# Kernel optimization log

Measured on AMD Instinct MI355X. Metric: run time of the kernel, lower is better.

## Reference

```python
import jax, jax.numpy as jnp
import numpy as np

NC = 80
CONF = 0.25
IOU_T = 0.45
MAX_DET = 100
ATTN_RES = 14
NUM_BASE = 5
TOPK = 1024          # candidate pre-filter (EfficientNMS-style)
SCALE = 0.25         # spatial_scale of ROIAlign


def setup_inputs() -> dict:
    key = jax.random.key(0)
    k1, k2, k3, k4 = jax.random.split(key, 4)
    B, A = 4, 25200
    test = jax.random.uniform(k1, (B, A, 5 + NC), dtype=jnp.float32)
    # scale boxes to image coords: cx,cy in [0,608), w,h in [0,120)
    box_scale = jnp.concatenate([jnp.array([608., 608., 120., 120.], jnp.float32),
                                 jnp.ones(1 + NC, jnp.float32)])
    test = test * box_scale
    attn = jax.random.normal(k2, (B, A, NUM_BASE * ATTN_RES * ATTN_RES), dtype=jnp.float32)
    bases = jax.random.normal(k3, (B, NUM_BASE - 1, 160, 160), dtype=jnp.float32)
    sem = jax.random.normal(k4, (B, 1, 160, 160), dtype=jnp.float32)
    return {"test": test, "attn": attn, "bases": bases, "sem": sem}


def _iou_matrix(b):
    # b: [K,4] xyxy
    area = jnp.clip(b[:, 2] - b[:, 0], 0) * jnp.clip(b[:, 3] - b[:, 1], 0)
    lt = jnp.maximum(b[:, None, :2], b[None, :, :2])
    rb = jnp.minimum(b[:, None, 2:], b[None, :, 2:])
    wh = jnp.clip(rb - lt, 0)
    inter = wh[..., 0] * wh[..., 1]
    return inter / (area[:, None] + area[None, :] - inter + 1e-9)


def _nms_single(boxes, scores):
    # boxes [A,4], scores [A,NC]. Class-aware greedy NMS over top-K candidates.
    flat = scores.reshape(-1)
    flat = jnp.where(flat > CONF, flat, -jnp.inf)
    top_s, top_i = jax.lax.top_k(flat, TOPK)
    anchor = top_i // NC
    cls = top_i % NC
    cb = boxes[anchor]                                   # [K,4]
    sup = (_iou_matrix(cb) > IOU_T) & (cls[:, None] == cls[None, :])

    def step(valid, _):
        s = jnp.where(valid, top_s, -jnp.inf)
        j = jnp.argmax(s)
        ok = jnp.isfinite(s[j])
        nv = (valid & ~sup[j]).at[j].set(False)
        return jnp.where(ok, nv, valid), (j, ok)

    _, (sel, selok) = jax.lax.scan(step, jnp.isfinite(top_s), None, length=MAX_DET)
    dboxes = jnp.where(selok[:, None], cb[sel], 0.)
    dscores = jnp.where(selok, top_s[sel], 0.)
    dcls = jnp.where(selok, cls[sel], 0).astype(jnp.int32)
    didx = jnp.where(selok, anchor[sel], 0).astype(jnp.int32)
    return selok.sum().astype(jnp.int32), dboxes, dscores, dcls, didx


def _roi_align(feat, rois, bidx, oh, ow, scale):
    # feat [B,C,H,W], rois [N,4] xyxy (input coords), half_pixel transform,
    # avg mode, 1 sample/bin (adaptive ratio = 1 here since bins < 1 px).
    N = rois.shape[0]
    B, C, H, W = feat.shape
    x1 = rois[:, 0] * scale - 0.5
    y1 = rois[:, 1] * scale - 0.5
    x2 = rois[:, 2] * scale - 0.5
    y2 = rois[:, 3] * scale - 0.5
    ys = y1[:, None] + (jnp.arange(oh, dtype=feat.dtype) + 0.5) * ((y2 - y1) / oh)[:, None]
    xs = x1[:, None] + (jnp.arange(ow, dtype=feat.dtype) + 0.5) * ((x2 - x1) / ow)[:, None]

    def axis(coord, dim):
        valid = (coord > -1.0) & (coord < dim)
        c = jnp.clip(coord, 0.0, dim - 1.0)
        lo = jnp.floor(c)
        hi = jnp.clip(lo + 1, 0, dim - 1)
        return lo.astype(jnp.int32), hi.astype(jnp.int32), c - lo, valid

    y0, y1i, wy, vy = axis(ys, H)
    x0, x1i, wx, vx = axis(xs, W)
    featn = feat[bidx]                                   # [N,C,H,W]
    n = jnp.arange(N)[:, None, None]

    def g(Y, X):  # -> [N,oh,ow,C]
        return featn[n, :, Y[:, :, None], X[:, None, :]]

    wy_ = wy[:, :, None, None]
    wx_ = wx[:, None, :, None]
    val = (g(y0, x0) * (1 - wy_) * (1 - wx_) + g(y0, x1i) * (1 - wy_) * wx_
           + g(y1i, x0) * wy_ * (1 - wx_) + g(y1i, x1i) * wy_ * wx_)
    val = jnp.where((vy[:, :, None] & vx[:, None, :])[..., None], val, 0.)
    return jnp.transpose(val, (0, 3, 1, 2))                # [N,C,oh,ow]


def _forward(test, attn, bases_in, sem):
    bases = jnp.concatenate([bases_in, sem], axis=1)       # [B,5,H,W]
    conv = jnp.array([[1, 0, 1, 0], [0, 1, 0, 1],
                      [-0.5, 0, 0.5, 0], [0, -0.5, 0, 0.5]], test.dtype)
    boxes = test[:, :, :4] @ conv                          # cxcywh -> xyxy
    scores = test[:, :, 5:5 + NC] * test[:, :, 4:5]
    _, dboxes, dscores, dcls, didx = jax.vmap(_nms_single)(boxes, scores)
    B, P, H, W = bases.shape
    bidx = jnp.repeat(jnp.arange(B), MAX_DET)              # [B*D]
    box_i = didx.reshape(-1)
    sel_boxes = boxes[bidx, box_i]                         # [N,4]
    sel_masks = attn[bidx, box_i]                          # [N,980]
    pooled = _roi_align(bases, sel_boxes, bidx, H, W, SCALE)  # [N,5,H,W]
    coeffs = sel_masks.reshape(-1, NUM_BASE, ATTN_RES, ATTN_RES)
    coeffs = jax.image.resize(coeffs, (coeffs.shape[0], NUM_BASE, H, W), 'linear')
    coeffs = jax.nn.softmax(coeffs, axis=1)
    masks = jax.nn.sigmoid((pooled * coeffs).sum(axis=1).reshape(B, MAX_DET, H * W))
    return jnp.concatenate([dboxes, dscores[..., None],
                            dcls.astype(test.dtype)[..., None], masks], axis=-1)


def reference(test, attn, bases, sem):
    return _forward(test, attn, bases, sem)
```

## Files before the change

### kernel.cpp

```cpp
#include <hip/hip_runtime.h>
#include <stdint.h>

#define B_   4
#define A_   25200
#define NC_  80
#define ROW_ 85
#define ATT_ 980
#define MAXDET_ 100
#define TOPK_ 1024
#define CAP_  4096
#define OUTSTRIDE_ 25606
#define HW_ 160
#define HWHW_ 25600
#define CONF_ 0.25f
#define IOUT_ 0.45f

#define WS_HIST 0
#define WS_CNT  4096
#define WS_TB   4160
#define WS_NTOP 4224
#define WS_CAND 8192
#define WS_TOPV 139264
#define WS_TOPA 155648
#define WS_TOPC 172032
#define WS_CB   188416
#define WS_SUP  253952
#define WS_DETA 778240

typedef unsigned long long u64;
typedef unsigned u32;

__global__ void k_clear(char* w) {
    int i = blockIdx.x * 256 + threadIdx.x;
    if (i < 1028) ((u32*)w)[i] = 0u;
}

__global__ void k_hist(const float* __restrict__ test, char* __restrict__ w) {
    int b = blockIdx.y;
    __shared__ u32 h[256];
    if (threadIdx.x < 256) h[threadIdx.x] = 0u;
    __syncthreads();
    const int total = A_ * NC_;
    for (int e = blockIdx.x * 256 + threadIdx.x; e < total; e += 128 * 256) {
        u32 a = (u32)e / 80u;
        u32 c = (u32)e - a * 80u;
        const float* row = test + ((size_t)b * A_ + a) * ROW_;
        float s = row[5 + c] * row[4];
        if (s > CONF_) {
            u32 key = __float_as_uint(s);
            int wb = (int)(key >> 17) - 7936;
            wb = wb < 0 ? 0 : (wb > 255 ? 255 : wb);
            atomicAdd(&h[wb], 1u);
        }
    }
    __syncthreads();
    u32* hist = (u32*)(w + WS_HIST);
    if (threadIdx.x < 256 && h[threadIdx.x]) atomicAdd(&hist[b * 256 + threadIdx.x], h[threadIdx.x]);
}

__global__ void k_thresh(char* w) {
    if (threadIdx.x < B_) {
        int b = threadIdx.x;
        const u32* h = (const u32*)(w + WS_HIST) + b * 256;
        u32 cum = 0; int wtb = 0;
        for (int i = 255; i >= 0; --i) {
            cum += h[i];
            if (cum >= TOPK_) { wtb = i; break; }
        }
        ((int*)(w + WS_TB))[b] = wtb;
    }
}

__global__ void k_collect(const float* __restrict__ test, char* __restrict__ w) {
    int b = blockIdx.y;
    int wtb = ((const int*)(w + WS_TB))[b];
    u32* cnt = (u32*)(w + WS_CNT);
    u64* cand = (u64*)(w + WS_CAND);
    const int total = A_ * NC_;
    for (int e = blockIdx.x * 256 + threadIdx.x; e < total; e += 128 * 256) {
        u32 a = (u32)e / 80u;
        u32 c = (u32)e - a * 80u;
        const float* row = test + ((size_t)b * A_ + a) * ROW_;
        float s = row[5 + c] * row[4];
        if (s > CONF_) {
            u32 key = __float_as_uint(s);
            int wb = (int)(key >> 17) - 7936;
            wb = wb < 0 ? 0 : (wb > 255 ? 255 : wb);
            if (wb >= wtb) {
                u32 pos = atomicAdd(&cnt[b], 1u);
                if (pos < CAP_)
                    cand[(size_t)b * CAP_ + pos] = ((u64)key << 32) | (u64)(0xFFFFFFFFu - (u32)e);
            }
        }
    }
}

__global__ __launch_bounds__(1024) void k_sort(const float* __restrict__ test, char* __restrict__ w) {
    int b = blockIdx.x;
    __shared__ u64 sm[CAP_];
    u32 cnt = ((const u32*)(w + WS_CNT))[b];
    int n = cnt < CAP_ ? (int)cnt : CAP_;
    const u64* cand = (const u64*)(w + WS_CAND) + (size_t)b * CAP_;
    for (int i = threadIdx.x; i < CAP_; i += 1024) sm[i] = (i < n) ? cand[i] : 0ull;
    __syncthreads();
    for (int k = 2; k <= CAP_; k <<= 1) {
        for (int j = k >> 1; j > 0; j >>= 1) {
            for (int t = threadIdx.x; t < CAP_; t += 1024) {
                int ixj = t ^ j;
                if (ixj > t) {
                    u64 a = sm[t], c = sm[ixj];
                    bool desc = ((t & k) == 0);
                    if (desc ? (a < c) : (a > c)) { sm[t] = c; sm[ixj] = a; }
                }
            }
            __syncthreads();
        }
    }
    int ntop = n < TOPK_ ? n : TOPK_;
    if (threadIdx.x == 0) ((int*)(w + WS_NTOP))[b] = ntop;
    if (threadIdx.x < TOPK_) {
        int i = threadIdx.x;
        float* topv = (float*)(w + WS_TOPV);
        int* topa = (int*)(w + WS_TOPA);
        int* topc = (int*)(w + WS_TOPC);
        float4* cb = (float4*)(w + WS_CB);
        if (i < ntop) {
            u64 v = sm[i];
            u32 key = (u32)(v >> 32);
            u32 idx = 0xFFFFFFFFu - (u32)(v & 0xFFFFFFFFull);
            u32 anchor = idx / 80u;
            u32 cls = idx - anchor * 80u;
            const float* tr = test + ((size_t)b * A_ + anchor) * ROW_;
            float cx = tr[0], cy = tr[1], ww = tr[2], hh = tr[3];
            float4 box;
            box.x = cx - 0.5f * ww; box.y = cy - 0.5f * hh;
            box.z = cx + 0.5f * ww; box.w = cy + 0.5f * hh;
            topv[b * TOPK_ + i] = __uint_as_float(key);
            topa[b * TOPK_ + i] = (int)anchor;
            topc[b * TOPK_ + i] = (int)cls;
            cb[b * TOPK_ + i] = box;
        } else {
            topv[b * TOPK_ + i] = 0.f;
            topa[b * TOPK_ + i] = 0;
            topc[b * TOPK_ + i] = 0;
            cb[b * TOPK_ + i] = make_float4(0.f, 0.f, 0.f, 0.f);
        }
    }
}

__device__ __forceinline__ bool sup_pair(float4 a, float4 b, int ca, int cbb) {
#pragma clang fp contract(off)
    if (ca != cbb) return false;
    float areaA = fmaxf(a.z - a.x, 0.f) * fmaxf(a.w - a.y, 0.f);
    float areaB = fmaxf(b.z - b.x, 0.f) * fmaxf(b.w - b.y, 0.f);
    float ltx = fmaxf(a.x, b.x), lty = fmaxf(a.y, b.y);
    float rbx = fminf(a.z, b.z), rby = fminf(a.w, b.w);
    float iw = fmaxf(rbx - ltx, 0.f), ih = fmaxf(rby - lty, 0.f);
    float inter = iw * ih;
    float iou = inter / (((areaA + areaB) - inter) + 1e-9f);
    return iou > IOUT_;
}

__global__ void k_sup(char* __restrict__ w) {
    int b = blockIdx.y;
    int t = blockIdx.x * 256 + threadIdx.x;
    int row = t >> 4, chunk = t & 15;
    const float4* cb = (const float4*)(w + WS_CB) + (size_t)b * TOPK_;
    const int* topc = (const int*)(w + WS_TOPC) + (size_t)b * TOPK_;
    float4 rb = cb[row];
    int rc = topc[row];
    u64 bits = 0ull;
    int base = chunk * 64;
    for (int cc = 0; cc < 64; ++cc) {
        if (sup_pair(rb, cb[base + cc], rc, topc[base + cc])) bits |= (1ull << cc);
    }
    ((u64*)(w + WS_SUP))[((size_t)b * TOPK_ + row) * 16 + chunk] = bits;
}

__global__ void k_nms(char* __restrict__ w, float* __restrict__ out) {
    int b = blockIdx.x;
    int lane = threadIdx.x;
    int ntop = ((const int*)(w + WS_NTOP))[b];
    const u64* sup = (const u64*)(w + WS_SUP);
    __shared__ int selA[MAXDET_];
    __shared__ int okA[MAXDET_];
    u32 valid = 0u;
    for (int t = 0; t < 16; ++t)
        if (lane * 16 + t < ntop) valid |= (1u << t);
    for (int k = 0; k < MAXDET_; ++k) {
        u64 bal = __ballot(valid != 0u);
        if (bal == 0ull) {
            if (lane == 0) { selA[k] = 0; okA[k] = 0; }
            continue;
        }
        int L = __ffsll(bal) - 1;
        u32 vL = (u32)__shfl((int)valid, L);
        int j = L * 16 + (__ffs(vL & 0xFFFFu) - 1);
        u64 chunk = sup[((size_t)b * TOPK_ + j) * 16 + (lane >> 2)];
        u32 s16 = (u32)(chunk >> ((lane & 3) * 16)) & 0xFFFFu;
        valid &= ~s16;
        if (lane == L) valid &= ~(1u << (j & 15));
        if (lane == 0) { selA[k] = j; okA[k] = 1; }
    }
    __syncthreads();
    const float* topv = (const float*)(w + WS_TOPV) + (size_t)b * TOPK_;
    const int* topa = (const int*)(w + WS_TOPA) + (size_t)b * TOPK_;
    const int* topc = (const int*)(w + WS_TOPC) + (size_t)b * TOPK_;
    const float4* cb = (const float4*)(w + WS_CB) + (size_t)b * TOPK_;
    int* deta = (int*)(w + WS_DETA);
    for (int k = lane; k < MAXDET_; k += 64) {
        int ok = okA[k], s = selA[k];
        float b0 = 0, b1 = 0, b2 = 0, b3 = 0, sc = 0; int cls_ = 0, anc = 0;
        if (ok) {
            float4 bb = cb[s];
            b0 = bb.x; b1 = bb.y; b2 = bb.z; b3 = bb.w;
            sc = topv[s]; cls_ = topc[s]; anc = topa[s];
        }
        size_t o = ((size_t)(b * MAXDET_ + k)) * OUTSTRIDE_;
        out[o + 0] = b0; out[o + 1] = b1; out[o + 2] = b2; out[o + 3] = b3;
        out[o + 4] = sc; out[o + 5] = (float)cls_;
        deta[b * MAXDET_ + k] = anc;
    }
}

__global__ __launch_bounds__(256) void k_mask(const float* __restrict__ test, const float* __restrict__ attn,
                       const float* __restrict__ bases, const float* __restrict__ sem,
                       const char* __restrict__ w, float* __restrict__ out) {
    int roi = blockIdx.x;
    int by = blockIdx.y;
    int b = roi / MAXDET_;
    int anchor = ((const int*)(w + WS_DETA))[roi];
    const float* t = test + ((size_t)b * A_ + anchor) * ROW_;
    float cx = t[0], cy = t[1], ww = t[2], hh = t[3];
    float bx1 = cx - 0.5f * ww, by1 = cy - 0.5f * hh;
    float bx2 = cx + 0.5f * ww, by2 = cy + 0.5f * hh;
    float rx1 = bx1 * 0.25f - 0.5f, ry1 = by1 * 0.25f - 0.5f;
    float rx2 = bx2 * 0.25f - 0.5f, ry2 = by2 * 0.25f - 0.5f;
    float xstep = (rx2 - rx1) / 160.f, ystep = (ry2 - ry1) / 160.f;

    __shared__ float XR[5 * 8 * 160];
    __shared__ float CXR[5 * 4 * 160];
    __shared__ float att[ATT_];
    __shared__ int   sxlo[HW_], sxhi[HW_];
    __shared__ float sxw[HW_], sxvF[HW_];
    __shared__ int   rzlo[HW_];
    __shared__ float rzw[HW_];
    __shared__ int   yloA[20], yhiA[20], cyloA[20], cyhiA[20];
    __shared__ float ywA[20], cwyA[20], yvF[20];
    __shared__ int rminS, crminS;

    int tid = threadIdx.x;
    const float* arow = attn + ((size_t)b * A_ + anchor) * ATT_;
    for (int i = tid; i < ATT_; i += 256) att[i] = arow[i];
    if (tid < HW_) {
        float coord = rx1 + (tid + 0.5f) * xstep;
        sxvF[tid] = (coord > -1.0f && coord < 160.0f) ? 1.f : 0.f;
        float c = fminf(fmaxf(coord, 0.f), 159.f);
        float lo = floorf(c);
        sxlo[tid] = (int)lo; sxhi[tid] = min((int)lo + 1, 159); sxw[tid] = c - lo;
        float f = (tid + 0.5f) * (14.f / 160.f) - 0.5f;
        float rc = fminf(fmaxf(f, 0.f), 13.f);
        float rlo = floorf(rc);
        rzlo[tid] = (int)rlo; rzw[tid] = rc - rlo;
    }
    __syncthreads();
    if (tid < 20) {
        int yg = by * 20 + tid;
        float coord = ry1 + (yg + 0.5f) * ystep;
        yvF[tid] = (coord > -1.0f && coord < 160.0f) ? 1.f : 0.f;
        float c = fminf(fmaxf(coord, 0.f), 159.f);
        float lo = floorf(c);
        yloA[tid] = (int)lo; yhiA[tid] = min((int)lo + 1, 159); ywA[tid] = c - lo;
        cyloA[tid] = rzlo[yg]; cwyA[tid] = rzw[yg]; cyhiA[tid] = min(rzlo[yg] + 1, 13);
    }
    __syncthreads();
    if (tid == 0) {
        int rm = 159, cm = 13;
        for (int i = 0; i < 20; ++i) { rm = min(rm, yloA[i]); cm = min(cm, cyloA[i]); }
        rminS = rm; crminS = cm;
    }
    __syncthreads();
    int rmin = rminS, crmin = crminS;

    const float* bp[5];
    bp[0] = bases + ((size_t)b * 4 + 0) * HWHW_;
    bp[1] = bases + ((size_t)b * 4 + 1) * HWHW_;
    bp[2] = bases + ((size_t)b * 4 + 2) * HWHW_;
    bp[3] = bases + ((size_t)b * 4 + 3) * HWHW_;
    bp[4] = sem + (size_t)b * HWHW_;

    for (int idx = tid; idx < 5 * 8 * 160; idx += 256) {
        int c = idx / (8 * 160);
        int rem = idx - c * (8 * 160);
        int r = rem / 160;
        int x = rem - r * 160;
        int row = min(rmin + r, 159);
        const float* pb = bp[c] + row * 160;
        float wx = sxw[x];
        XR[idx] = pb[sxlo[x]] * (1.f - wx) + pb[sxhi[x]] * wx;
    }
    for (int idx = tid; idx < 5 * 4 * 160; idx += 256) {
        int c = idx / (4 * 160);
        int rem = idx - c * (4 * 160);
        int rr = rem / 160;
        int x = rem - rr * 160;
        int row = min(crmin + rr, 13);
        const float* pa = att + c * 196 + row * 14;
        int xl = rzlo[x]; int xh = min(xl + 1, 13); float wxc = rzw[x];
        CXR[idx] = pa[xl] * (1.f - wxc) + pa[xh] * wxc;
    }
    __syncthreads();

    size_t obase = (size_t)roi * OUTSTRIDE_ + 6 + (size_t)by * 20 * HW_;
    for (int g = tid; g < 800; g += 256) {
        int yl = g / 40;
        int x4 = (g - yl * 40) * 4;
        float wy = ywA[yl], vy = yvF[yl], cwy = cwyA[yl];
        int rlo = min(max(yloA[yl] - rmin, 0), 7);
        int rhi = min(max(yhiA[yl] - rmin, 0), 7);
        int clo = min(max(cyloA[yl] - crmin, 0), 3);
        int chi = min(max(cyhiA[yl] - crmin, 0), 3);
        float p4[5][4], cf4[5][4];
#pragma unroll
        for (int c = 0; c < 5; ++c) {
            float4 a = *(const float4*)&XR[(c * 8 + rlo) * 160 + x4];
            float4 bq = *(const float4*)&XR[(c * 8 + rhi) * 160 + x4];
            p4[c][0] = a.x * (1.f - wy) + bq.x * wy;
            p4[c][1] = a.y * (1.f - wy) + bq.y * wy;
            p4[c][2] = a.z * (1.f - wy) + bq.z * wy;
            p4[c][3] = a.w * (1.f - wy) + bq.w * wy;
            float4 ca = *(const float4*)&CXR[(c * 4 + clo) * 160 + x4];
            float4 cbq = *(const float4*)&CXR[(c * 4 + chi) * 160 + x4];
            cf4[c][0] = ca.x * (1.f - cwy) + cbq.x * cwy;
            cf4[c][1] = ca.y * (1.f - cwy) + cbq.y * cwy;
            cf4[c][2] = ca.z * (1.f - cwy) + cbq.z * cwy;
            cf4[c][3] = ca.w * (1.f - cwy) + cbq.w * cwy;
        }
        float4 vx4 = *(const float4*)&sxvF[x4];
        float vx[4] = { vx4.x, vx4.y, vx4.z, vx4.w };
        float res[4];
#pragma unroll
        for (int i = 0; i < 4; ++i) {
            float v = vx[i] * vy;
            float se = 0.f, dot = 0.f;
#pragma unroll
            for (int c = 0; c < 5; ++c) {
                float e = __expf(cf4[c][i]);
                se += e;
                dot += p4[c][i] * e;
            }
            float r = v * dot / se;
            res[i] = 1.f / (1.f + __expf(-r));
        }
        float2* o2 = (float2*)(out + obase + (size_t)yl * HW_ + x4);
        o2[0] = make_float2(res[0], res[1]);
        o2[1] = make_float2(res[2], res[3]);
    }
}

extern "C" void kernel_launch(void* const* d_in, const int* in_sizes, int n_in,
                              void* d_out, int out_size, void* d_ws, size_t ws_size,
                              hipStream_t stream) {
    const float* test = (const float*)d_in[0];
    const float* attn = (const float*)d_in[1];
    const float* bases = (const float*)d_in[2];
    const float* sem = (const float*)d_in[3];
    float* out = (float*)d_out;
    char* w = (char*)d_ws;

    k_clear<<<5, 256, 0, stream>>>(w);
    k_hist<<<dim3(128, B_), 256, 0, stream>>>(test, w);
    k_thresh<<<1, 64, 0, stream>>>(w);
    k_collect<<<dim3(128, B_), 256, 0, stream>>>(test, w);
    k_sort<<<B_, 1024, 0, stream>>>(test, w);
    k_sup<<<dim3(64, B_), 256, 0, stream>>>(w);
    k_nms<<<B_, 64, 0, stream>>>(w, out);
    k_mask<<<dim3(B_ * MAXDET_, 8), 256, 0, stream>>>(test, attn, bases, sem, w, out);
}
```

Before: 735.0 us.

## Split candidates into sure and boundary sets, sort only the boundary bucket

The threshold computation moves into the last block of the histogram kernel using a completion ticket, which removes one launch. Candidates strictly above the threshold bucket go to an unsorted 'sure' list, and only the boundary bucket is bitonic-sorted, padded to a power of two. Because the sure list is no longer ordered, the NMS kernel now finds the highest-scoring valid candidate with a wave-wide max reduction over packed keys instead of taking the first set bit. The mask kernel also shrinks its staged row buffer from 8 to 6 rows, which assumes that many rows cover each 20-row band.

```diff
diff --git a/kernel.cpp b/kernel.cpp
--- a/kernel.cpp
+++ b/kernel.cpp
@@ -8,7 +8,8 @@
 #define ATT_ 980
 #define MAXDET_ 100
 #define TOPK_ 1024
-#define CAP_  4096
+#define SURECAP_ 1024
+#define BNDCAP_  4096
 #define OUTSTRIDE_ 25606
 #define HW_ 160
 #define HWHW_ 25600
@@ -16,30 +17,78 @@
 #define IOUT_ 0.45f
 
 #define WS_HIST 0
-#define WS_CNT  4096
-#define WS_TB   4160
-#define WS_NTOP 4224
-#define WS_CAND 8192
-#define WS_TOPV 139264
-#define WS_TOPA 155648
-#define WS_TOPC 172032
-#define WS_CB   188416
-#define WS_SUP  253952
-#define WS_DETA 778240
+#define WS_DONE 4096
+#define WS_SCNT 4160
+#define WS_BCNT 4224
+#define WS_TB   4288
+#define WS_NTOP 4352
+#define WS_SURE 8192
+#define WS_BND  40960
+#define WS_KEY  172032
+#define WS_TOPV 204800
+#define WS_TOPA 221184
+#define WS_TOPC 237568
+#define WS_CB   253952
+#define WS_SUP  319488
+#define WS_DETA 843776
 
 typedef unsigned long long u64;
 typedef unsigned u32;
 
+__device__ __forceinline__ int bucket_of(u32 key) {
+    int wb = (int)(key >> 17) - 7936;
+    return wb < 0 ? 0 : (wb > 255 ? 255 : wb);
+}
+
 __global__ void k_clear(char* w) {
-    int i = blockIdx.x * 256 + threadIdx.x;
-    if (i < 1028) ((u32*)w)[i] = 0u;
+    for (int i = threadIdx.x; i < 1072; i += 1024) ((u32*)w)[i] = 0u;
 }
 
 __global__ void k_hist(const float* __restrict__ test, char* __restrict__ w) {
     int b = blockIdx.y;
     __shared__ u32 h[256];
+    __shared__ u32 ticket;
     if (threadIdx.x < 256) h[threadIdx.x] = 0u;
     __syncthreads();
+    const int total = A_ * NC_;
+    for (int e = blockIdx.x * 256 + threadIdx.x; e < total; e += 128 * 256) {
+        u32 a = (u32)e / 80u;
+        u32 c = (u32)e - a * 80u;
+        const float* row = test + ((size_t)b * A_ + a) * ROW_;
+        float s = row[5 + c] * row[4];
+        if (s > CONF_) atomicAdd(&h[bucket_of(__float_as_uint(s))], 1u);
+    }
+    __syncthreads();
+    u32* hist = (u32*)(w + WS_HIST);
+    if (threadIdx.x < 256 && h[threadIdx.x]) atomicAdd(&hist[b * 256 + threadIdx.x], h[threadIdx.x]);
+    __threadfence();
+    __syncthreads();
+    if (threadIdx.x == 0) ticket = atomicAdd((u32*)(w + WS_DONE), 1u);
+    __syncthreads();
+    if (ticket == 128u * B_ - 1u) {
+        __shared__ u32 hh[B_ * 256];
+        for (int i = threadIdx.x; i < B_ * 256; i += 256)
+            hh[i] = atomicAdd(&hist[i], 0u);
+        __syncthreads();
+        if (threadIdx.x < B_) {
+            const u32* hb = hh + threadIdx.x * 256;
+            u32 cum = 0; int wtb = 0;
+            for (int i = 255; i >= 0; --i) {
+                cum += hb[i];
+                if (cum >= TOPK_) { wtb = i; break; }
+            }
+            ((int*)(w + WS_TB))[threadIdx.x] = wtb;
+        }
+    }
+}
+
+__global__ void k_collect(const float* __restrict__ test, char* __restrict__ w) {
+    int b = blockIdx.y;
+    int wtb = ((const int*)(w + WS_TB))[b];
+    u32* scnt = (u32*)(w + WS_SCNT);
+    u32* bcnt = (u32*)(w + WS_BCNT);
+    u64* sure = (u64*)(w + WS_SURE);
+    u64* bnd = (u64*)(w + WS_BND);
     const int total = A_ * NC_;
     for (int e = blockIdx.x * 256 + threadIdx.x; e < total; e += 128 * 256) {
         u32 a = (u32)e / 80u;
@@ -48,64 +97,35 @@
         float s = row[5 + c] * row[4];
         if (s > CONF_) {
             u32 key = __float_as_uint(s);
-            int wb = (int)(key >> 17) - 7936;
-            wb = wb < 0 ? 0 : (wb > 255 ? 255 : wb);
-            atomicAdd(&h[wb], 1u);
-        }
-    }
-    __syncthreads();
-    u32* hist = (u32*)(w + WS_HIST);
-    if (threadIdx.x < 256 && h[threadIdx.x]) atomicAdd(&hist[b * 256 + threadIdx.x], h[threadIdx.x]);
-}
-
-__global__ void k_thresh(char* w) {
-    if (threadIdx.x < B_) {
-        int b = threadIdx.x;
-        const u32* h = (const u32*)(w + WS_HIST) + b * 256;
-        u32 cum = 0; int wtb = 0;
-        for (int i = 255; i >= 0; --i) {
-            cum += h[i];
-            if (cum >= TOPK_) { wtb = i; break; }
-        }
-        ((int*)(w + WS_TB))[b] = wtb;
-    }
-}
-
-__global__ void k_collect(const float* __restrict__ test, char* __restrict__ w) {
-    int b = blockIdx.y;
-    int wtb = ((const int*)(w + WS_TB))[b];
-    u32* cnt = (u32*)(w + WS_CNT);
-    u64* cand = (u64*)(w + WS_CAND);
-    const int total = A_ * NC_;
-    for (int e = blockIdx.x * 256 + threadIdx.x; e < total; e += 128 * 256) {
-        u32 a = (u32)e / 80u;
-        u32 c = (u32)e - a * 80u;
-        const float* row = test + ((size_t)b * A_ + a) * ROW_;
-        float s = row[5 + c] * row[4];
-        if (s > CONF_) {
-            u32 key = __float_as_uint(s);
-            int wb = (int)(key >> 17) - 7936;
-            wb = wb < 0 ? 0 : (wb > 255 ? 255 : wb);
+            int wb = bucket_of(key);
             if (wb >= wtb) {
-                u32 pos = atomicAdd(&cnt[b], 1u);
-                if (pos < CAP_)
-                    cand[(size_t)b * CAP_ + pos] = ((u64)key << 32) | (u64)(0xFFFFFFFFu - (u32)e);
+                u64 packed = ((u64)key << 32) | (u64)(0xFFFFFFFFu - (u32)e);
+                if (wb > wtb) {
+                    u32 pos = atomicAdd(&scnt[b], 1u);
+                    if (pos < SURECAP_) sure[(size_t)b * SURECAP_ + pos] = packed;
+                } else {
+                    u32 pos = atomicAdd(&bcnt[b], 1u);
+                    if (pos < BNDCAP_) bnd[(size_t)b * BNDCAP_ + pos] = packed;
+                }
             }
         }
     }
 }
 
-__global__ __launch_bounds__(1024) void k_sort(const float* __restrict__ test, char* __restrict__ w) {
+__global__ __launch_bounds__(1024) void k_bsort(const float* __restrict__ test, char* __restrict__ w) {
     int b = blockIdx.x;
-    __shared__ u64 sm[CAP_];
-    u32 cnt = ((const u32*)(w + WS_CNT))[b];
-    int n = cnt < CAP_ ? (int)cnt : CAP_;
-    const u64* cand = (const u64*)(w + WS_CAND) + (size_t)b * CAP_;
-    for (int i = threadIdx.x; i < CAP_; i += 1024) sm[i] = (i < n) ? cand[i] : 0ull;
-    __syncthreads();
-    for (int k = 2; k <= CAP_; k <<= 1) {
+    __shared__ u64 sm[BNDCAP_];
+    u32 ns_raw = ((const u32*)(w + WS_SCNT))[b];
+    u32 nb_raw = ((const u32*)(w + WS_BCNT))[b];
+    int ns = ns_raw < SURECAP_ ? (int)ns_raw : SURECAP_;
+    int nb = nb_raw < BNDCAP_ ? (int)nb_raw : BNDCAP_;
+    int p = 2; while (p < nb) p <<= 1;
+    const u64* bnd = (const u64*)(w + WS_BND) + (size_t)b * BNDCAP_;
+    for (int i = threadIdx.x; i < p; i += 1024) sm[i] = (i < nb) ? bnd[i] : 0ull;
+    __syncthreads();
+    for (int k = 2; k <= p; k <<= 1) {
         for (int j = k >> 1; j > 0; j >>= 1) {
-            for (int t = threadIdx.x; t < CAP_; t += 1024) {
+            for (int t = threadIdx.x; t < p; t += 1024) {
                 int ixj = t ^ j;
                 if (ixj > t) {
                     u64 a = sm[t], c = sm[ixj];
@@ -116,35 +136,39 @@
             __syncthreads();
         }
     }
-    int ntop = n < TOPK_ ? n : TOPK_;
+    int m = TOPK_ - ns; if (m > nb) m = nb;
+    int ntop = ns + m;
     if (threadIdx.x == 0) ((int*)(w + WS_NTOP))[b] = ntop;
-    if (threadIdx.x < TOPK_) {
-        int i = threadIdx.x;
-        float* topv = (float*)(w + WS_TOPV);
-        int* topa = (int*)(w + WS_TOPA);
-        int* topc = (int*)(w + WS_TOPC);
-        float4* cb = (float4*)(w + WS_CB);
-        if (i < ntop) {
-            u64 v = sm[i];
-            u32 key = (u32)(v >> 32);
-            u32 idx = 0xFFFFFFFFu - (u32)(v & 0xFFFFFFFFull);
-            u32 anchor = idx / 80u;
-            u32 cls = idx - anchor * 80u;
-            const float* tr = test + ((size_t)b * A_ + anchor) * ROW_;
-            float cx = tr[0], cy = tr[1], ww = tr[2], hh = tr[3];
-            float4 box;
-            box.x = cx - 0.5f * ww; box.y = cy - 0.5f * hh;
-            box.z = cx + 0.5f * ww; box.w = cy + 0.5f * hh;
-            topv[b * TOPK_ + i] = __uint_as_float(key);
-            topa[b * TOPK_ + i] = (int)anchor;
-            topc[b * TOPK_ + i] = (int)cls;
-            cb[b * TOPK_ + i] = box;
-        } else {
-            topv[b * TOPK_ + i] = 0.f;
-            topa[b * TOPK_ + i] = 0;
-            topc[b * TOPK_ + i] = 0;
-            cb[b * TOPK_ + i] = make_float4(0.f, 0.f, 0.f, 0.f);
-        }
+    const u64* sure = (const u64*)(w + WS_SURE) + (size_t)b * SURECAP_;
+    int i = threadIdx.x;
+    u64 v = 0ull;
+    if (i < ns) v = sure[i];
+    else if (i < ntop) v = sm[i - ns];
+    u64* keyo = (u64*)(w + WS_KEY);
+    float* topv = (float*)(w + WS_TOPV);
+    int* topa = (int*)(w + WS_TOPA);
+    int* topc = (int*)(w + WS_TOPC);
+    float4* cb = (float4*)(w + WS_CB);
+    keyo[(size_t)b * TOPK_ + i] = v;
+    if (v) {
+        u32 key = (u32)(v >> 32);
+        u32 idx = 0xFFFFFFFFu - (u32)(v & 0xFFFFFFFFull);
+        u32 anchor = idx / 80u;
+        u32 cls = idx - anchor * 80u;
+        const float* tr = test + ((size_t)b * A_ + anchor) * ROW_;
+        float cx = tr[0], cy = tr[1], ww = tr[2], hh = tr[3];
+        float4 box;
+        box.x = cx - 0.5f * ww; box.y = cy - 0.5f * hh;
+        box.z = cx + 0.5f * ww; box.w = cy + 0.5f * hh;
+        topv[b * TOPK_ + i] = __uint_as_float(key);
+        topa[b * TOPK_ + i] = (int)anchor;
+        topc[b * TOPK_ + i] = (int)cls;
+        cb[b * TOPK_ + i] = box;
+    } else {
+        topv[b * TOPK_ + i] = 0.f;
+        topa[b * TOPK_ + i] = 0;
+        topc[b * TOPK_ + i] = 0;
+        cb[b * TOPK_ + i] = make_float4(0.f, 0.f, 0.f, 0.f);
     }
 }
 
@@ -181,25 +205,45 @@
     int b = blockIdx.x;
     int lane = threadIdx.x;
     int ntop = ((const int*)(w + WS_NTOP))[b];
+    const u64* keys = (const u64*)(w + WS_KEY) + (size_t)b * TOPK_;
     const u64* sup = (const u64*)(w + WS_SUP);
     __shared__ int selA[MAXDET_];
     __shared__ int okA[MAXDET_];
+    u64 k16[16];
+#pragma unroll
+    for (int t = 0; t < 16; ++t) k16[t] = keys[lane * 16 + t];
     u32 valid = 0u;
+#pragma unroll
     for (int t = 0; t < 16; ++t)
         if (lane * 16 + t < ntop) valid |= (1u << t);
     for (int k = 0; k < MAXDET_; ++k) {
-        u64 bal = __ballot(valid != 0u);
-        if (bal == 0ull) {
+        u64 lbest = 0ull; int lslot = -1;
+#pragma unroll
+        for (int t = 0; t < 16; ++t) {
+            u64 cand = ((valid >> t) & 1u) ? k16[t] : 0ull;
+            if (cand > lbest) { lbest = cand; lslot = t; }
+        }
+        u64 best = lbest;
+#pragma unroll
+        for (int off = 32; off > 0; off >>= 1) {
+            u64 o = (u64)__shfl_xor((long long)best, off);
+            best = o > best ? o : best;
+        }
+        if (best == 0ull) {
             if (lane == 0) { selA[k] = 0; okA[k] = 0; }
             continue;
         }
-        int L = __ffsll(bal) - 1;
-        u32 vL = (u32)__shfl((int)valid, L);
-        int j = L * 16 + (__ffs(vL & 0xFFFFu) - 1);
+        int jc = (lbest == best) ? lane * 16 + lslot : 0x7FFFFFFF;
+#pragma unroll
+        for (int off = 32; off > 0; off >>= 1) {
+            int o = __shfl_xor(jc, off);
+            jc = o < jc ? o : jc;
+        }
+        int j = jc;
         u64 chunk = sup[((size_t)b * TOPK_ + j) * 16 + (lane >> 2)];
         u32 s16 = (u32)(chunk >> ((lane & 3) * 16)) & 0xFFFFu;
         valid &= ~s16;
-        if (lane == L) valid &= ~(1u << (j & 15));
+        if ((j >> 4) == lane) valid &= ~(1u << (j & 15));
         if (lane == 0) { selA[k] = j; okA[k] = 1; }
     }
     __syncthreads();
@@ -232,13 +276,11 @@
     int anchor = ((const int*)(w + WS_DETA))[roi];
     const float* t = test + ((size_t)b * A_ + anchor) * ROW_;
     float cx = t[0], cy = t[1], ww = t[2], hh = t[3];
-    float bx1 = cx - 0.5f * ww, by1 = cy - 0.5f * hh;
-    float bx2 = cx + 0.5f * ww, by2 = cy + 0.5f * hh;
-    float rx1 = bx1 * 0.25f - 0.5f, ry1 = by1 * 0.25f - 0.5f;
-    float rx2 = bx2 * 0.25f - 0.5f, ry2 = by2 * 0.25f - 0.5f;
+    float rx1 = (cx - 0.5f * ww) * 0.25f - 0.5f, ry1 = (cy - 0.5f * hh) * 0.25f - 0.5f;
+    float rx2 = (cx + 0.5f * ww) * 0.25f - 0.5f, ry2 = (cy + 0.5f * hh) * 0.25f - 0.5f;
     float xstep = (rx2 - rx1) / 160.f, ystep = (ry2 - ry1) / 160.f;
 
-    __shared__ float XR[5 * 8 * 160];
+    __shared__ float XR[5 * 6 * 160];
     __shared__ float CXR[5 * 4 * 160];
     __shared__ float att[ATT_];
     __shared__ int   sxlo[HW_], sxhi[HW_];
@@ -289,9 +331,9 @@
     bp[3] = bases + ((size_t)b * 4 + 3) * HWHW_;
     bp[4] = sem + (size_t)b * HWHW_;
 
-    for (int idx = tid; idx < 5 * 8 * 160; idx += 256) {
-        int c = idx / (8 * 160);
-        int rem = idx - c * (8 * 160);
+    for (int idx = tid; idx < 5 * 6 * 160; idx += 256) {
+        int c = idx / (6 * 160);
+        int rem = idx - c * (6 * 160);
         int r = rem / 160;
         int x = rem - r * 160;
         int row = min(rmin + r, 159);
@@ -316,15 +358,15 @@
         int yl = g / 40;
         int x4 = (g - yl * 40) * 4;
         float wy = ywA[yl], vy = yvF[yl], cwy = cwyA[yl];
-        int rlo = min(max(yloA[yl] - rmin, 0), 7);
-        int rhi = min(max(yhiA[yl] - rmin, 0), 7);
+        int rlo = min(max(yloA[yl] - rmin, 0), 5);
+        int rhi = min(max(yhiA[yl] - rmin, 0), 5);
         int clo = min(max(cyloA[yl] - crmin, 0), 3);
         int chi = min(max(cyhiA[yl] - crmin, 0), 3);
         float p4[5][4], cf4[5][4];
 #pragma unroll
         for (int c = 0; c < 5; ++c) {
-            float4 a = *(const float4*)&XR[(c * 8 + rlo) * 160 + x4];
-            float4 bq = *(const float4*)&XR[(c * 8 + rhi) * 160 + x4];
+            float4 a = *(const float4*)&XR[(c * 6 + rlo) * 160 + x4];
+            float4 bq = *(const float4*)&XR[(c * 6 + rhi) * 160 + x4];
             p4[c][0] = a.x * (1.f - wy) + bq.x * wy;
             p4[c][1] = a.y * (1.f - wy) + bq.y * wy;
             p4[c][2] = a.z * (1.f - wy) + bq.z * wy;
@@ -368,11 +410,10 @@
     float* out = (float*)d_out;
     char* w = (char*)d_ws;
 
-    k_clear<<<5, 256, 0, stream>>>(w);
+    k_clear<<<1, 1024, 0, stream>>>(w);
     k_hist<<<dim3(128, B_), 256, 0, stream>>>(test, w);
-    k_thresh<<<1, 64, 0, stream>>>(w);
     k_collect<<<dim3(128, B_), 256, 0, stream>>>(test, w);
-    k_sort<<<B_, 1024, 0, stream>>>(test, w);
+    k_bsort<<<B_, 1024, 0, stream>>>(test, w);
     k_sup<<<dim3(64, B_), 256, 0, stream>>>(w);
     k_nms<<<B_, 64, 0, stream>>>(w, out);
     k_mask<<<dim3(B_ * MAXDET_, 8), 256, 0, stream>>>(test, attn, bases, sem, w, out);
```

Result: slower. 775.7 us (+5.6%).
